# Optimization experiments

Measured on AMD Instinct MI355X. Metric: run time of the kernel, lower is better.

## Reference

```python
import jax, jax.numpy as jnp
import numpy as np

B, H, L, D = 2, 16, 2048, 128


def setup_inputs() -> dict:
    key = jax.random.key(0)
    kq, kk, kv = jax.random.split(key, 3)
    q = jax.random.normal(kq, (B, H, L, D), dtype=jnp.float32)
    k = jax.random.normal(kk, (B, H, L, D), dtype=jnp.float32)
    v = jax.random.normal(kv, (B, H, L, D), dtype=jnp.float32)
    return {"q": q, "k": k, "v": v}


def reference(q, k, v):
    # Causal prefill attention (flash_attn_varlen_func / SDPA is_causal=True path).
    # q, k, v: [B, H, L, D]; scale = 1/sqrt(D) as in the fallback and constructor.
    Lq = q.shape[2]
    Dh = q.shape[3]
    scale = 1.0 / jnp.sqrt(jnp.asarray(Dh, q.dtype))
    scores = jnp.einsum('bhqd,bhkd->bhqk', q, k) * scale  # [B,H,Lq,Lk]
    causal = jnp.tril(jnp.ones((Lq, Lq), dtype=bool))      # [Lq,Lk]
    scores = jnp.where(causal, scores, jnp.finfo(q.dtype).min)
    probs = jax.nn.softmax(scores, axis=-1)
    return jnp.einsum('bhqk,bhkd->bhqd', probs, v)          # [B,H,Lq,D]
```

## Files before the change

### kernel.cpp

```cpp
#include <hip/hip_runtime.h>
#include <hip/hip_bf16.h>
#include <stdint.h>


#define BB 2
#define HH 16
#define LL 2048
#define DD 128

typedef float f32x4 __attribute__((ext_vector_type(4)));
typedef __bf16 bf16x8 __attribute__((ext_vector_type(8)));
typedef __bf16 bf16x2t __attribute__((ext_vector_type(2)));

union Frag16 {
    uint4    u;
    bf16x8   b;
    uint16_t s[8];
    uint32_t w32[4];
};

__device__ inline uint32_t pk2bf(float x, float y) {
    bf16x2t v;
    v.x = (__bf16)x;
    v.y = (__bf16)y;
    return __builtin_bit_cast(uint32_t, v);
}

__device__ inline uint16_t f2bf(float x) {
    uint32_t u = __builtin_bit_cast(uint32_t, x);
    u += 0x7fffu + ((u >> 16) & 1u);
    return (uint16_t)(u >> 16);
}

__device__ inline float fast_exp2(float x) {
#if __has_builtin(__builtin_amdgcn_exp2f)
    return __builtin_amdgcn_exp2f(x);
#else
    return exp2f(x);
#endif
}

__constant__ uint8_t QT[32] = {
    31, 16,  1, 14,   18, 29, 12,  3,    4, 11, 26, 21,    9,  6, 23, 24,
     0, 15, 30, 17,   13,  2, 19, 28,   27, 20,  5, 10,   22, 25,  8,  7};

__global__ __launch_bounds__(256) void conv_kv(
    const float* __restrict__ Kg, const float* __restrict__ Vg,
    uint4* __restrict__ Kf, uint4* __restrict__ Vf)
{
    const int bid = blockIdx.x;
    const int t   = threadIdx.x;
    if (bid < 2048) {
        const int unit = bid;
        #pragma unroll
        for (int i = 0; i < 2; ++i) {
            const int local = t + i * 256;
            const int tile  = unit * 2 + (local >> 8);
            const int c     = local & 255;
            const int ds = c >> 6, quad = (c >> 4) & 3, n16 = c & 15;
            const float* p = Kg + ((size_t)tile * 16 + n16) * DD + ds * 32 + quad * 8;
            float4 a = *(const float4*)p;
            float4 b = *(const float4*)(p + 4);
            Frag16 f;
            f.w32[0] = pk2bf(a.x, a.y); f.w32[1] = pk2bf(a.z, a.w);
            f.w32[2] = pk2bf(b.x, b.y); f.w32[3] = pk2bf(b.z, b.w);
            Kf[(size_t)tile * 256 + c] = f.u;
        }
    } else {
        const int g = bid - 2048;
        const int n16 = t & 15, dt = (t >> 4) & 7, quadH = t >> 7;
        #pragma unroll
        for (int qi = 0; qi < 2; ++qi) {
            const int quad = quadH + 2 * qi;
            const float* base = Vg + ((size_t)g * 32 + quad * 8) * DD + dt * 16 + n16;
            float v[8];
            #pragma unroll
            for (int j = 0; j < 8; ++j) v[j] = base[(size_t)j * DD];
            Frag16 f;
            f.w32[0] = pk2bf(v[0], v[1]); f.w32[1] = pk2bf(v[2], v[3]);
            f.w32[2] = pk2bf(v[4], v[5]); f.w32[3] = pk2bf(v[6], v[7]);
            Vf[(size_t)g * 512 + dt * 64 + quad * 16 + n16] = f.u;
        }
    }
}

__global__ __launch_bounds__(256, 2) void fa_main(
    const float* __restrict__ Qg, const uint4* __restrict__ Kf,
    const uint4* __restrict__ Vf, float* __restrict__ Og)
{
    __shared__ __align__(16) uint16_t Plds[4][16 * 72];

    const int tid  = threadIdx.x;
    const int lane = tid & 63;
    const int w    = tid >> 6;
    const int n16  = lane & 15;
    const int quad = lane >> 4;

    const int i     = blockIdx.x;
    const int xcd   = i & 7;
    const int j     = i >> 3;
    const int k4    = j & 3;
    const int bh_lo = (j >> 2) & 3;
    const int hi    = (j >> 4) & 1;
    const int a4    = j >> 5;
    const int qtile = QT[hi * 16 + a4 * 4 + k4];
    const int bh    = xcd * 4 + bh_lo;

    constexpr float kC   = 0.08838834764831845f * 1.4426950408889634f;
    constexpr float kOff = -16.0f * 1.4426950408889634f;

    const uint4* kpb = Kf + (size_t)(bh * 128) * 256 + lane;
    const uint4* vpb = Vf + (size_t)(bh * 64) * 512 + lane;
    float* Oh = Og + (size_t)bh * LL * DD;

    const int q0     = qtile * 64;
    const int q_base = q0 + w * 16;

    Frag16 qf[4];
    {
        const float* qrow = Qg + ((size_t)bh * LL + q_base + n16) * DD;
        #pragma unroll
        for (int ds = 0; ds < 4; ++ds) {
            const int d0 = ds * 32 + quad * 8;
            float4 a = *(const float4*)(qrow + d0);
            float4 b = *(const float4*)(qrow + d0 + 4);
            qf[ds].w32[0] = pk2bf(a.x, a.y); qf[ds].w32[1] = pk2bf(a.z, a.w);
            qf[ds].w32[2] = pk2bf(b.x, b.y); qf[ds].w32[3] = pk2bf(b.z, b.w);
        }
    }

    f32x4 oacc[8];
    #pragma unroll
    for (int dt = 0; dt < 8; ++dt) oacc[dt] = (f32x4)0.0f;
    float lpart = 0.0f;

    const int ntiles = qtile + 1;

    for (int t = 0; t < ntiles; ++t) {
        const int kv0 = t << 6;
        const uint4* kp = kpb + (size_t)(kv0 >> 4) * 256;
        const uint4* vp = vpb + (size_t)(kv0 >> 5) * 512;

        f32x4 sacc[4] = {(f32x4)0.0f, (f32x4)0.0f, (f32x4)0.0f, (f32x4)0.0f};
        {
            Frag16 kf[2][4];
            #pragma unroll
            for (int kt = 0; kt < 2; ++kt)
                #pragma unroll
                for (int ds = 0; ds < 4; ++ds) kf[kt][ds].u = kp[kt * 256 + ds * 64];
            __builtin_amdgcn_s_setprio(1);
            #pragma unroll
            for (int ds = 0; ds < 4; ++ds) {
                sacc[0] = __builtin_amdgcn_mfma_f32_16x16x32_bf16(kf[0][ds].b, qf[ds].b, sacc[0], 0, 0, 0);
                sacc[1] = __builtin_amdgcn_mfma_f32_16x16x32_bf16(kf[1][ds].b, qf[ds].b, sacc[1], 0, 0, 0);
            }
            __builtin_amdgcn_s_setprio(0);
            #pragma unroll
            for (int kt = 0; kt < 2; ++kt)
                #pragma unroll
                for (int ds = 0; ds < 4; ++ds) kf[kt][ds].u = kp[(kt + 2) * 256 + ds * 64];
            __builtin_amdgcn_s_setprio(1);
            #pragma unroll
            for (int ds = 0; ds < 4; ++ds) {
                sacc[2] = __builtin_amdgcn_mfma_f32_16x16x32_bf16(kf[0][ds].b, qf[ds].b, sacc[2], 0, 0, 0);
                sacc[3] = __builtin_amdgcn_mfma_f32_16x16x32_bf16(kf[1][ds].b, qf[ds].b, sacc[3], 0, 0, 0);
            }
            __builtin_amdgcn_s_setprio(0);
        }

        Frag16 vf[2][8];
        #pragma unroll
        for (int h = 0; h < 2; ++h)
            #pragma unroll
            for (int dt = 0; dt < 8; ++dt) vf[h][dt].u = vp[h * 512 + dt * 64];

        if (kv0 + 63 > q_base) {
            const int qg_ = q_base + n16;
            #pragma unroll
            for (int kt = 0; kt < 4; ++kt) {
                const int kvg = kv0 + kt * 16 + quad * 4;
                #pragma unroll
                for (int r = 0; r < 4; ++r)
                    if (kvg + r > qg_) sacc[kt][r] = -1e30f;
            }
        }

        #pragma unroll
        for (int kt = 0; kt < 4; ++kt) {
            float p0 = fast_exp2(fmaf(sacc[kt][0], kC, kOff));
            float p1 = fast_exp2(fmaf(sacc[kt][1], kC, kOff));
            float p2 = fast_exp2(fmaf(sacc[kt][2], kC, kOff));
            float p3 = fast_exp2(fmaf(sacc[kt][3], kC, kOff));
            lpart += (p0 + p1) + (p2 + p3);
            uint2 pw;
            pw.x = pk2bf(p0, p1);
            pw.y = pk2bf(p2, p3);
            *(uint2*)&Plds[w][n16 * 72 + kt * 16 + quad * 4] = pw;
        }

        #pragma unroll
        for (int h = 0; h < 2; ++h) {
            Frag16 pf;
            pf.u = *(const uint4*)&Plds[w][n16 * 72 + h * 32 + quad * 8];
            __builtin_amdgcn_s_setprio(1);
            #pragma unroll
            for (int dt = 0; dt < 8; ++dt)
                oacc[dt] = __builtin_amdgcn_mfma_f32_16x16x32_bf16(
                    pf.b, vf[h][dt].b, oacc[dt], 0, 0, 0);
            __builtin_amdgcn_s_setprio(0);
        }
    }

    float lsum = lpart;
    lsum += __shfl_xor(lsum, 16);
    lsum += __shfl_xor(lsum, 32);
    #pragma unroll
    for (int r = 0; r < 4; ++r) {
        const float inv = 1.0f / __shfl(lsum, quad * 4 + r);
        float* orow = Oh + (size_t)(q_base + quad * 4 + r) * DD + n16;
        #pragma unroll
        for (int dt = 0; dt < 8; ++dt)
            orow[dt * 16] = oacc[dt][r] * inv;
    }
}

__global__ __launch_bounds__(256) void fa_fallback(
    const float* __restrict__ Qg, const float* __restrict__ Kg,
    const float* __restrict__ Vg, float* __restrict__ Og)
{
    __shared__ uint4 Klds[32 * 16];
    __shared__ uint4 Vlds[128 * 4];
    __shared__ __align__(16) uint16_t Plds[4][32 * 40];

    const int tid  = threadIdx.x;
    const int lane = tid & 63;
    const int w    = tid >> 6;
    const int n16  = lane & 15;
    const int quad = lane >> 4;

    const int bh     = blockIdx.y;
    const int q0     = (gridDim.x - 1 - blockIdx.x) * 128;
    const int q_base = q0 + w * 32;

    const size_t base = (size_t)bh * LL * DD;
    const float* Qh = Qg + base;
    const float* Kh = Kg + base;
    const float* Vh = Vg + base;
    float*       Oh = Og + base;

    constexpr float kC = 0.08838834764831845f * 1.4426950408889634f;

    Frag16 qf[2][4];
    #pragma unroll
    for (int qt = 0; qt < 2; ++qt) {
        const float* qrow = Qh + (size_t)(q_base + qt * 16 + n16) * DD;
        #pragma unroll
        for (int ds = 0; ds < 4; ++ds) {
            const int d0 = ds * 32 + quad * 8;
            float4 a = *(const float4*)(qrow + d0);
            float4 b = *(const float4*)(qrow + d0 + 4);
            Frag16 f;
            f.s[0] = f2bf(a.x); f.s[1] = f2bf(a.y); f.s[2] = f2bf(a.z); f.s[3] = f2bf(a.w);
            f.s[4] = f2bf(b.x); f.s[5] = f2bf(b.y); f.s[6] = f2bf(b.z); f.s[7] = f2bf(b.w);
            qf[qt][ds] = f;
        }
    }

    f32x4 oacc[2][8];
    #pragma unroll
    for (int qt = 0; qt < 2; ++qt)
        #pragma unroll
        for (int dt = 0; dt < 8; ++dt) oacc[qt][dt] = (f32x4)0.0f;
    float mrow[2] = {-1e30f, -1e30f};
    float lrow[2] = {0.0f, 0.0f};

    const int ntiles = q0 / 32 + 4;

    for (int t = 0; t < ntiles; ++t) {
        const int kv0 = t * 32;
        __syncthreads();
        #pragma unroll
        for (int iu = 0; iu < 2; ++iu) {
            const int cid = tid + iu * 256;
            const int r = cid >> 4, c = cid & 15;
            const float* src = Kh + (size_t)(kv0 + r) * DD + c * 8;
            float4 a = *(const float4*)src;
            float4 b = *(const float4*)(src + 4);
            Frag16 f;
            f.s[0] = f2bf(a.x); f.s[1] = f2bf(a.y); f.s[2] = f2bf(a.z); f.s[3] = f2bf(a.w);
            f.s[4] = f2bf(b.x); f.s[5] = f2bf(b.y); f.s[6] = f2bf(b.z); f.s[7] = f2bf(b.w);
            Klds[r * 16 + (c ^ (r & 7))] = f.u;
        }
        #pragma unroll
        for (int iu = 0; iu < 2; ++iu) {
            const int cid = tid + iu * 256;
            const int d = cid >> 2, ch = cid & 3;
            const float* src = Vh + (size_t)(kv0 + ch * 8) * DD + d;
            Frag16 f;
            #pragma unroll
            for (int j = 0; j < 8; ++j) f.s[j] = f2bf(src[(size_t)j * DD]);
            Vlds[d * 4 + (ch ^ ((d >> 1) & 3))] = f.u;
        }
        __syncthreads();

        if (kv0 > q_base + 31) continue;

        f32x4 sacc[2][2];
        #pragma unroll
        for (int kt = 0; kt < 2; ++kt)
            #pragma unroll
            for (int qt = 0; qt < 2; ++qt) sacc[kt][qt] = (f32x4)0.0f;

        #pragma unroll
        for (int ds = 0; ds < 4; ++ds) {
            Frag16 kfr[2];
            #pragma unroll
            for (int kt = 0; kt < 2; ++kt) {
                const int r = kt * 16 + n16;
                const int c = ds * 4 + quad;
                kfr[kt].u = Klds[r * 16 + (c ^ (r & 7))];
            }
            #pragma unroll
            for (int kt = 0; kt < 2; ++kt)
                #pragma unroll
                for (int qt = 0; qt < 2; ++qt)
                    sacc[kt][qt] = __builtin_amdgcn_mfma_f32_16x16x32_bf16(
                        kfr[kt].b, qf[qt][ds].b, sacc[kt][qt], 0, 0, 0);
        }

        if (kv0 + 31 > q_base) {
            #pragma unroll
            for (int kt = 0; kt < 2; ++kt) {
                const int kvg = kv0 + kt * 16 + quad * 4;
                #pragma unroll
                for (int qt = 0; qt < 2; ++qt) {
                    const int qg_ = q_base + qt * 16 + n16;
                    #pragma unroll
                    for (int r = 0; r < 4; ++r)
                        if (kvg + r > qg_) sacc[kt][qt][r] = -1e30f;
                }
            }
        }

        #pragma unroll
        for (int qt = 0; qt < 2; ++qt) {
            float mt = sacc[0][qt][0];
            #pragma unroll
            for (int kt = 0; kt < 2; ++kt)
                #pragma unroll
                for (int r = 0; r < 4; ++r) mt = fmaxf(mt, sacc[kt][qt][r]);
            mt = fmaxf(mt, __shfl_xor(mt, 16));
            mt = fmaxf(mt, __shfl_xor(mt, 32));
            const float mnew  = fmaxf(mrow[qt], mt);
            const float alpha = exp2f((mrow[qt] - mnew) * kC);
            mrow[qt] = mnew;

            float ls = 0.0f;
            uint16_t* prow = &Plds[w][(qt * 16 + n16) * 40];
            #pragma unroll
            for (int kt = 0; kt < 2; ++kt)
                #pragma unroll
                for (int r = 0; r < 4; ++r) {
                    const float p = exp2f((sacc[kt][qt][r] - mnew) * kC);
                    ls += p;
                    prow[kt * 16 + quad * 4 + r] = f2bf(p);
                }
            ls += __shfl_xor(ls, 16);
            ls += __shfl_xor(ls, 32);
            lrow[qt] = lrow[qt] * alpha + ls;

            #pragma unroll
            for (int r = 0; r < 4; ++r) {
                const float ar = __shfl(alpha, quad * 4 + r);
                #pragma unroll
                for (int dt = 0; dt < 8; ++dt) oacc[qt][dt][r] *= ar;
            }
        }

        Frag16 pfr[2];
        #pragma unroll
        for (int qt = 0; qt < 2; ++qt)
            pfr[qt].u = *(const uint4*)&Plds[w][(qt * 16 + n16) * 40 + quad * 8];
        #pragma unroll
        for (int dt = 0; dt < 8; ++dt) {
            const int d = dt * 16 + n16;
            Frag16 vfr;
            vfr.u = Vlds[d * 4 + (quad ^ ((d >> 1) & 3))];
            #pragma unroll
            for (int qt = 0; qt < 2; ++qt)
                oacc[qt][dt] = __builtin_amdgcn_mfma_f32_16x16x32_bf16(
                    pfr[qt].b, vfr.b, oacc[qt][dt], 0, 0, 0);
        }
    }

    #pragma unroll
    for (int qt = 0; qt < 2; ++qt) {
        #pragma unroll
        for (int r = 0; r < 4; ++r) {
            const float lr  = __shfl(lrow[qt], quad * 4 + r);
            const float inv = 1.0f / lr;
            const int row = q_base + qt * 16 + quad * 4 + r;
            float* orow = Oh + (size_t)row * DD + n16;
            #pragma unroll
            for (int dt = 0; dt < 8; ++dt)
                orow[dt * 16] = oacc[qt][dt][r] * inv;
        }
    }
}

extern "C" void kernel_launch(void* const* d_in, const int* in_sizes, int n_in,
                              void* d_out, int out_size, void* d_ws, size_t ws_size,
                              hipStream_t stream) {
    const float* q = (const float*)d_in[0];
    const float* k = (const float*)d_in[1];
    const float* v = (const float*)d_in[2];
    float* o = (float*)d_out;

    const size_t TENS = (size_t)BB * HH * LL * DD * 2;
    if (ws_size >= 2 * TENS) {
        uint4* Kf = (uint4*)d_ws;
        uint4* Vf = (uint4*)((char*)d_ws + TENS);
        conv_kv<<<dim3(4096), dim3(256), 0, stream>>>(k, v, Kf, Vf);
        fa_main<<<dim3(1024), dim3(256), 0, stream>>>(q, Kf, Vf, o);
    } else {
        fa_fallback<<<dim3(16, BB * HH), dim3(256), 0, stream>>>(q, k, v, o);
    }
}
```

Before: 208.1 us.

## Split KV range across wave pairs and pair causal q-tiles for balance

Each block now handles two 32-row query tiles, pair and 63-pair, so causal work is balanced per block. This replaces the QT permutation table. Within a tile, two waves split the KV tiles odd/even and merge partial outputs and row sums through shared memory before the final write. The goal is better load balance and shorter per-wave serial KV loops, at the cost of extra LDS traffic, two barriers per phase, and smaller 32-wide KV steps.

```diff
diff --git a/kernel.cpp b/kernel.cpp
--- a/kernel.cpp
+++ b/kernel.cpp
@@ -39,10 +39,6 @@
     return exp2f(x);
 #endif
 }
-
-__constant__ uint8_t QT[32] = {
-    31, 16,  1, 14,   18, 29, 12,  3,    4, 11, 26, 21,    9,  6, 23, 24,
-     0, 15, 30, 17,   13,  2, 19, 28,   27, 20,  5, 10,   22, 25,  8,  7};
 
 __global__ __launch_bounds__(256) void conv_kv(
     const float* __restrict__ Kg, const float* __restrict__ Vg,
@@ -88,23 +84,23 @@
     const float* __restrict__ Qg, const uint4* __restrict__ Kf,
     const uint4* __restrict__ Vf, float* __restrict__ Og)
 {
-    __shared__ __align__(16) uint16_t Plds[4][16 * 72];
-
-    const int tid  = threadIdx.x;
-    const int lane = tid & 63;
-    const int w    = tid >> 6;
-    const int n16  = lane & 15;
-    const int quad = lane >> 4;
+    __shared__ __align__(16) uint16_t Plds[4][16 * 40];
+    __shared__ float Obuf[2][16 * 132];
+    __shared__ float Lbuf[2][16];
+
+    const int tid   = threadIdx.x;
+    const int lane  = tid & 63;
+    const int w     = tid >> 6;
+    const int n16   = lane & 15;
+    const int quad  = lane >> 4;
+    const int qhalf = w & 1;
+    const int kvway = w >> 1;
 
     const int i     = blockIdx.x;
     const int xcd   = i & 7;
     const int j     = i >> 3;
-    const int k4    = j & 3;
-    const int bh_lo = (j >> 2) & 3;
-    const int hi    = (j >> 4) & 1;
-    const int a4    = j >> 5;
-    const int qtile = QT[hi * 16 + a4 * 4 + k4];
-    const int bh    = xcd * 4 + bh_lo;
+    const int pair  = j & 31;
+    const int bh    = xcd * 4 + (j >> 5);
 
     constexpr float kC   = 0.08838834764831845f * 1.4426950408889634f;
     constexpr float kOff = -16.0f * 1.4426950408889634f;
@@ -113,36 +109,38 @@
     const uint4* vpb = Vf + (size_t)(bh * 64) * 512 + lane;
     float* Oh = Og + (size_t)bh * LL * DD;
 
-    const int q0     = qtile * 64;
-    const int q_base = q0 + w * 16;
-
-    Frag16 qf[4];
-    {
-        const float* qrow = Qg + ((size_t)bh * LL + q_base + n16) * DD;
-        #pragma unroll
-        for (int ds = 0; ds < 4; ++ds) {
-            const int d0 = ds * 32 + quad * 8;
-            float4 a = *(const float4*)(qrow + d0);
-            float4 b = *(const float4*)(qrow + d0 + 4);
-            qf[ds].w32[0] = pk2bf(a.x, a.y); qf[ds].w32[1] = pk2bf(a.z, a.w);
-            qf[ds].w32[2] = pk2bf(b.x, b.y); qf[ds].w32[3] = pk2bf(b.z, b.w);
-        }
-    }
-
-    f32x4 oacc[8];
     #pragma unroll
-    for (int dt = 0; dt < 8; ++dt) oacc[dt] = (f32x4)0.0f;
-    float lpart = 0.0f;
-
-    const int ntiles = qtile + 1;
-
-    for (int t = 0; t < ntiles; ++t) {
-        const int kv0 = t << 6;
-        const uint4* kp = kpb + (size_t)(kv0 >> 4) * 256;
-        const uint4* vp = vpb + (size_t)(kv0 >> 5) * 512;
-
-        f32x4 sacc[4] = {(f32x4)0.0f, (f32x4)0.0f, (f32x4)0.0f, (f32x4)0.0f};
+    for (int phase = 0; phase < 2; ++phase) {
+        const int P32    = phase ? 63 - pair : pair;
+        const int q0     = P32 * 32;
+        const int q_base = q0 + qhalf * 16;
+
+        Frag16 qf[4];
         {
+            const float* qrow = Qg + ((size_t)bh * LL + q_base + n16) * DD;
+            #pragma unroll
+            for (int ds = 0; ds < 4; ++ds) {
+                const int d0 = ds * 32 + quad * 8;
+                float4 a = *(const float4*)(qrow + d0);
+                float4 b = *(const float4*)(qrow + d0 + 4);
+                qf[ds].w32[0] = pk2bf(a.x, a.y); qf[ds].w32[1] = pk2bf(a.z, a.w);
+                qf[ds].w32[2] = pk2bf(b.x, b.y); qf[ds].w32[3] = pk2bf(b.z, b.w);
+            }
+        }
+
+        f32x4 oacc[8];
+        #pragma unroll
+        for (int dt = 0; dt < 8; ++dt) oacc[dt] = (f32x4)0.0f;
+        float lpart = 0.0f;
+
+        const int nt = P32 + 1;
+
+        for (int t = kvway; t < nt; t += 2) {
+            const int kv0 = t << 5;
+            const uint4* kp = kpb + (size_t)(t * 2) * 256;
+            const uint4* vp = vpb + (size_t)t * 512;
+
+            f32x4 sacc[2] = {(f32x4)0.0f, (f32x4)0.0f};
             Frag16 kf[2][4];
             #pragma unroll
             for (int kt = 0; kt < 2; ++kt)
@@ -155,72 +153,71 @@
                 sacc[1] = __builtin_amdgcn_mfma_f32_16x16x32_bf16(kf[1][ds].b, qf[ds].b, sacc[1], 0, 0, 0);
             }
             __builtin_amdgcn_s_setprio(0);
-            #pragma unroll
-            for (int kt = 0; kt < 2; ++kt)
-                #pragma unroll
-                for (int ds = 0; ds < 4; ++ds) kf[kt][ds].u = kp[(kt + 2) * 256 + ds * 64];
-            __builtin_amdgcn_s_setprio(1);
-            #pragma unroll
-            for (int ds = 0; ds < 4; ++ds) {
-                sacc[2] = __builtin_amdgcn_mfma_f32_16x16x32_bf16(kf[0][ds].b, qf[ds].b, sacc[2], 0, 0, 0);
-                sacc[3] = __builtin_amdgcn_mfma_f32_16x16x32_bf16(kf[1][ds].b, qf[ds].b, sacc[3], 0, 0, 0);
-            }
-            __builtin_amdgcn_s_setprio(0);
-        }
-
-        Frag16 vf[2][8];
-        #pragma unroll
-        for (int h = 0; h < 2; ++h)
-            #pragma unroll
-            for (int dt = 0; dt < 8; ++dt) vf[h][dt].u = vp[h * 512 + dt * 64];
-
-        if (kv0 + 63 > q_base) {
-            const int qg_ = q_base + n16;
-            #pragma unroll
-            for (int kt = 0; kt < 4; ++kt) {
-                const int kvg = kv0 + kt * 16 + quad * 4;
-                #pragma unroll
-                for (int r = 0; r < 4; ++r)
-                    if (kvg + r > qg_) sacc[kt][r] = -1e30f;
-            }
-        }
-
-        #pragma unroll
-        for (int kt = 0; kt < 4; ++kt) {
-            float p0 = fast_exp2(fmaf(sacc[kt][0], kC, kOff));
-            float p1 = fast_exp2(fmaf(sacc[kt][1], kC, kOff));
-            float p2 = fast_exp2(fmaf(sacc[kt][2], kC, kOff));
-            float p3 = fast_exp2(fmaf(sacc[kt][3], kC, kOff));
-            lpart += (p0 + p1) + (p2 + p3);
-            uint2 pw;
-            pw.x = pk2bf(p0, p1);
-            pw.y = pk2bf(p2, p3);
-            *(uint2*)&Plds[w][n16 * 72 + kt * 16 + quad * 4] = pw;
-        }
-
-        #pragma unroll
-        for (int h = 0; h < 2; ++h) {
+
+            Frag16 vf[8];
+            #pragma unroll
+            for (int dt = 0; dt < 8; ++dt) vf[dt].u = vp[dt * 64];
+
+            if (kv0 + 31 > q_base) {
+                const int qg_ = q_base + n16;
+                #pragma unroll
+                for (int kt = 0; kt < 2; ++kt) {
+                    const int kvg = kv0 + kt * 16 + quad * 4;
+                    #pragma unroll
+                    for (int r = 0; r < 4; ++r)
+                        if (kvg + r > qg_) sacc[kt][r] = -1e30f;
+                }
+            }
+
+            #pragma unroll
+            for (int kt = 0; kt < 2; ++kt) {
+                float p0 = fast_exp2(fmaf(sacc[kt][0], kC, kOff));
+                float p1 = fast_exp2(fmaf(sacc[kt][1], kC, kOff));
+                float p2 = fast_exp2(fmaf(sacc[kt][2], kC, kOff));
+                float p3 = fast_exp2(fmaf(sacc[kt][3], kC, kOff));
+                lpart += (p0 + p1) + (p2 + p3);
+                uint2 pw;
+                pw.x = pk2bf(p0, p1);
+                pw.y = pk2bf(p2, p3);
+                *(uint2*)&Plds[w][n16 * 40 + kt * 16 + quad * 4] = pw;
+            }
+
             Frag16 pf;
-            pf.u = *(const uint4*)&Plds[w][n16 * 72 + h * 32 + quad * 8];
+            pf.u = *(const uint4*)&Plds[w][n16 * 40 + quad * 8];
             __builtin_amdgcn_s_setprio(1);
             #pragma unroll
             for (int dt = 0; dt < 8; ++dt)
                 oacc[dt] = __builtin_amdgcn_mfma_f32_16x16x32_bf16(
-                    pf.b, vf[h][dt].b, oacc[dt], 0, 0, 0);
+                    pf.b, vf[dt].b, oacc[dt], 0, 0, 0);
             __builtin_amdgcn_s_setprio(0);
         }
-    }
-
-    float lsum = lpart;
-    lsum += __shfl_xor(lsum, 16);
-    lsum += __shfl_xor(lsum, 32);
-    #pragma unroll
-    for (int r = 0; r < 4; ++r) {
-        const float inv = 1.0f / __shfl(lsum, quad * 4 + r);
-        float* orow = Oh + (size_t)(q_base + quad * 4 + r) * DD + n16;
-        #pragma unroll
-        for (int dt = 0; dt < 8; ++dt)
-            orow[dt * 16] = oacc[dt][r] * inv;
+
+        float lsum = lpart;
+        lsum += __shfl_xor(lsum, 16);
+        lsum += __shfl_xor(lsum, 32);
+
+        if (kvway == 1) {
+            if (lane < 16) Lbuf[qhalf][lane] = lsum;
+            #pragma unroll
+            for (int dt = 0; dt < 8; ++dt)
+                #pragma unroll
+                for (int r = 0; r < 4; ++r)
+                    Obuf[qhalf][(quad * 4 + r) * 132 + dt * 16 + n16] = oacc[dt][r];
+        }
+        __syncthreads();
+        if (kvway == 0) {
+            lsum += Lbuf[qhalf][n16];
+            #pragma unroll
+            for (int r = 0; r < 4; ++r) {
+                const float inv = 1.0f / __shfl(lsum, quad * 4 + r);
+                const float* obr = &Obuf[qhalf][(quad * 4 + r) * 132 + n16];
+                float* orow = Oh + (size_t)(q_base + quad * 4 + r) * DD + n16;
+                #pragma unroll
+                for (int dt = 0; dt < 8; ++dt)
+                    orow[dt * 16] = (oacc[dt][r] + obr[dt * 16]) * inv;
+            }
+        }
+        __syncthreads();
     }
 }
 
```

After: 197.7 us. 5.0% less time.

## Stage K/V tiles into LDS with async double-buffered loads in attention

Applied to the files above, without the earlier changes.

The main attention kernel now copies each 32-key K/V tile into shared memory with global_load_lds, double-buffered across iterations, so the whole block shares one load instead of every wave fetching fragments from global memory. The step shrinks from 64 to 32 keys, and the row-sum is computed by an MFMA against a ones fragment instead of shuffles. Launch bounds go from 2 to 4 blocks per SM, and the V conversion kernel now transposes through shared memory so its global reads are coalesced. This adds per-step barriers and more LDS traffic, and the last-tile handling, where only waves 2-3 run the final compute, is delicate.

```diff
diff --git a/kernel.cpp b/kernel.cpp
--- a/kernel.cpp
+++ b/kernel.cpp
@@ -40,6 +40,12 @@
 #endif
 }
 
+__device__ __forceinline__ void stage16(const uint4* g, uint4* l) {
+    __builtin_amdgcn_global_load_lds(
+        (const __attribute__((address_space(1))) unsigned int*)g,
+        (__attribute__((address_space(3))) unsigned int*)l, 16, 0, 0);
+}
+
 __constant__ uint8_t QT[32] = {
     31, 16,  1, 14,   18, 29, 12,  3,    4, 11, 26, 21,    9,  6, 23, 24,
      0, 15, 30, 17,   13,  2, 19, 28,   27, 20,  5, 10,   22, 25,  8,  7};
@@ -48,6 +54,7 @@
     const float* __restrict__ Kg, const float* __restrict__ Vg,
     uint4* __restrict__ Kf, uint4* __restrict__ Vf)
 {
+    __shared__ uint16_t T[32 * 136];
     const int bid = blockIdx.x;
     const int t   = threadIdx.x;
     if (bid < 2048) {
@@ -68,27 +75,42 @@
         }
     } else {
         const int g = bid - 2048;
-        const int n16 = t & 15, dt = (t >> 4) & 7, quadH = t >> 7;
-        #pragma unroll
-        for (int qi = 0; qi < 2; ++qi) {
-            const int quad = quadH + 2 * qi;
-            const float* base = Vg + ((size_t)g * 32 + quad * 8) * DD + dt * 16 + n16;
-            float v[8];
-            #pragma unroll
-            for (int j = 0; j < 8; ++j) v[j] = base[(size_t)j * DD];
+        const float* Vsrc = Vg + (size_t)g * 32 * DD;
+        const int row = t >> 3;
+        const int cg  = (t & 7) * 16;
+        #pragma unroll
+        for (int k = 0; k < 4; ++k) {
+            float4 a = *(const float4*)(Vsrc + (size_t)row * DD + cg + k * 4);
+            uint2 pw;
+            pw.x = pk2bf(a.x, a.y);
+            pw.y = pk2bf(a.z, a.w);
+            *(uint2*)&T[row * 136 + cg + k * 4] = pw;
+        }
+        __syncthreads();
+        #pragma unroll
+        for (int e2 = 0; e2 < 2; ++e2) {
+            const int e   = t + e2 * 256;
+            const int dt  = e >> 6;
+            const int rem = e & 63;
+            const int qd  = rem >> 4;
+            const int nn  = rem & 15;
+            const int col = dt * 16 + nn;
             Frag16 f;
-            f.w32[0] = pk2bf(v[0], v[1]); f.w32[1] = pk2bf(v[2], v[3]);
-            f.w32[2] = pk2bf(v[4], v[5]); f.w32[3] = pk2bf(v[6], v[7]);
-            Vf[(size_t)g * 512 + dt * 64 + quad * 16 + n16] = f.u;
-        }
-    }
-}
-
-__global__ __launch_bounds__(256, 2) void fa_main(
+            #pragma unroll
+            for (int jj = 0; jj < 8; ++jj)
+                f.s[jj] = T[(qd * 8 + jj) * 136 + col];
+            Vf[(size_t)g * 512 + e] = f.u;
+        }
+    }
+}
+
+__global__ __launch_bounds__(256, 4) void fa_main(
     const float* __restrict__ Qg, const uint4* __restrict__ Kf,
     const uint4* __restrict__ Vf, float* __restrict__ Og)
 {
-    __shared__ __align__(16) uint16_t Plds[4][16 * 72];
+    __shared__ __align__(16) uint4 Klds[2][512];
+    __shared__ __align__(16) uint4 Vlds[2][512];
+    __shared__ __align__(16) uint16_t Plds[4][16 * 40];
 
     const int tid  = threadIdx.x;
     const int lane = tid & 63;
@@ -109,16 +131,18 @@
     constexpr float kC   = 0.08838834764831845f * 1.4426950408889634f;
     constexpr float kOff = -16.0f * 1.4426950408889634f;
 
-    const uint4* kpb = Kf + (size_t)(bh * 128) * 256 + lane;
-    const uint4* vpb = Vf + (size_t)(bh * 64) * 512 + lane;
     float* Oh = Og + (size_t)bh * LL * DD;
 
-    const int q0     = qtile * 64;
-    const int q_base = q0 + w * 16;
+    Frag16 onesf;
+    #pragma unroll
+    for (int z = 0; z < 8; ++z) onesf.s[z] = 0x3F80;
+
+    const int q0  = qtile * 64;
+    const int qw0 = q0 + w * 16;
 
     Frag16 qf[4];
     {
-        const float* qrow = Qg + ((size_t)bh * LL + q_base + n16) * DD;
+        const float* qrow = Qg + ((size_t)bh * LL + qw0 + n16) * DD;
         #pragma unroll
         for (int ds = 0; ds < 4; ++ds) {
             const int d0 = ds * 32 + quad * 8;
@@ -132,92 +156,103 @@
     f32x4 oacc[8];
     #pragma unroll
     for (int dt = 0; dt < 8; ++dt) oacc[dt] = (f32x4)0.0f;
-    float lpart = 0.0f;
-
-    const int ntiles = qtile + 1;
-
-    for (int t = 0; t < ntiles; ++t) {
-        const int kv0 = t << 6;
-        const uint4* kp = kpb + (size_t)(kv0 >> 4) * 256;
-        const uint4* vp = vpb + (size_t)(kv0 >> 5) * 512;
-
-        f32x4 sacc[4] = {(f32x4)0.0f, (f32x4)0.0f, (f32x4)0.0f, (f32x4)0.0f};
-        {
-            Frag16 kf[2][4];
-            #pragma unroll
-            for (int kt = 0; kt < 2; ++kt)
-                #pragma unroll
-                for (int ds = 0; ds < 4; ++ds) kf[kt][ds].u = kp[kt * 256 + ds * 64];
+    f32x4 lacc = (f32x4)0.0f;
+
+    const int ns = 2 * qtile + 2;
+
+    const uint4* sg = (w < 2 ? Kf + (size_t)(bh * 128) * 256
+                             : Vf + (size_t)(bh * 64) * 512)
+                      + (w & 1) * 256 + lane;
+    uint4* ldb = (w < 2 ? &Klds[0][0] : &Vlds[0][0]) + (w & 1) * 256;
+
+    auto STAGE = [&](int buf) {
+        uint4* ld = ldb + buf * 512;
+        #pragma unroll
+        for (int c = 0; c < 4; ++c) stage16(sg + c * 64, ld + c * 64);
+        sg += 512;
+    };
+
+    auto COMPUTE = [&](int buf, bool masked, int kv0) {
+        const uint4* Kl = &Klds[buf][0] + lane;
+        const uint4* Vl = &Vlds[buf][0] + lane;
+        f32x4 sacc[2];
+        sacc[0] = (f32x4)0.0f; sacc[1] = (f32x4)0.0f;
+        #pragma unroll
+        for (int kt = 0; kt < 2; ++kt) {
+            Frag16 kfr[4];
+            #pragma unroll
+            for (int ds = 0; ds < 4; ++ds) kfr[ds].u = Kl[kt * 256 + ds * 64];
             __builtin_amdgcn_s_setprio(1);
             #pragma unroll
-            for (int ds = 0; ds < 4; ++ds) {
-                sacc[0] = __builtin_amdgcn_mfma_f32_16x16x32_bf16(kf[0][ds].b, qf[ds].b, sacc[0], 0, 0, 0);
-                sacc[1] = __builtin_amdgcn_mfma_f32_16x16x32_bf16(kf[1][ds].b, qf[ds].b, sacc[1], 0, 0, 0);
-            }
+            for (int ds = 0; ds < 4; ++ds)
+                sacc[kt] = __builtin_amdgcn_mfma_f32_16x16x32_bf16(
+                    kfr[ds].b, qf[ds].b, sacc[kt], 0, 0, 0);
             __builtin_amdgcn_s_setprio(0);
-            #pragma unroll
-            for (int kt = 0; kt < 2; ++kt)
-                #pragma unroll
-                for (int ds = 0; ds < 4; ++ds) kf[kt][ds].u = kp[(kt + 2) * 256 + ds * 64];
-            __builtin_amdgcn_s_setprio(1);
-            #pragma unroll
-            for (int ds = 0; ds < 4; ++ds) {
-                sacc[2] = __builtin_amdgcn_mfma_f32_16x16x32_bf16(kf[0][ds].b, qf[ds].b, sacc[2], 0, 0, 0);
-                sacc[3] = __builtin_amdgcn_mfma_f32_16x16x32_bf16(kf[1][ds].b, qf[ds].b, sacc[3], 0, 0, 0);
-            }
-            __builtin_amdgcn_s_setprio(0);
-        }
-
-        Frag16 vf[2][8];
-        #pragma unroll
-        for (int h = 0; h < 2; ++h)
-            #pragma unroll
-            for (int dt = 0; dt < 8; ++dt) vf[h][dt].u = vp[h * 512 + dt * 64];
-
-        if (kv0 + 63 > q_base) {
-            const int qg_ = q_base + n16;
-            #pragma unroll
-            for (int kt = 0; kt < 4; ++kt) {
+        }
+        if (masked) {
+            const int qg_ = qw0 + n16;
+            #pragma unroll
+            for (int kt = 0; kt < 2; ++kt) {
                 const int kvg = kv0 + kt * 16 + quad * 4;
                 #pragma unroll
                 for (int r = 0; r < 4; ++r)
                     if (kvg + r > qg_) sacc[kt][r] = -1e30f;
             }
         }
-
-        #pragma unroll
-        for (int kt = 0; kt < 4; ++kt) {
+        uint16_t* pw = &Plds[w][n16 * 40];
+        #pragma unroll
+        for (int kt = 0; kt < 2; ++kt) {
             float p0 = fast_exp2(fmaf(sacc[kt][0], kC, kOff));
             float p1 = fast_exp2(fmaf(sacc[kt][1], kC, kOff));
             float p2 = fast_exp2(fmaf(sacc[kt][2], kC, kOff));
             float p3 = fast_exp2(fmaf(sacc[kt][3], kC, kOff));
-            lpart += (p0 + p1) + (p2 + p3);
-            uint2 pw;
-            pw.x = pk2bf(p0, p1);
-            pw.y = pk2bf(p2, p3);
-            *(uint2*)&Plds[w][n16 * 72 + kt * 16 + quad * 4] = pw;
-        }
-
-        #pragma unroll
-        for (int h = 0; h < 2; ++h) {
-            Frag16 pf;
-            pf.u = *(const uint4*)&Plds[w][n16 * 72 + h * 32 + quad * 8];
+            uint2 pw2;
+            pw2.x = pk2bf(p0, p1);
+            pw2.y = pk2bf(p2, p3);
+            *(uint2*)&pw[kt * 16 + quad * 4] = pw2;
+        }
+        Frag16 pf;
+        pf.u = *(const uint4*)&Plds[w][n16 * 40 + quad * 8];
+        __builtin_amdgcn_s_setprio(1);
+        lacc = __builtin_amdgcn_mfma_f32_16x16x32_bf16(pf.b, onesf.b, lacc, 0, 0, 0);
+        __builtin_amdgcn_s_setprio(0);
+        #pragma unroll
+        for (int half = 0; half < 2; ++half) {
+            Frag16 vf[4];
+            #pragma unroll
+            for (int dt = 0; dt < 4; ++dt)
+                vf[dt].u = Vl[(half * 4 + dt) * 64];
             __builtin_amdgcn_s_setprio(1);
             #pragma unroll
-            for (int dt = 0; dt < 8; ++dt)
-                oacc[dt] = __builtin_amdgcn_mfma_f32_16x16x32_bf16(
-                    pf.b, vf[h][dt].b, oacc[dt], 0, 0, 0);
+            for (int dt = 0; dt < 4; ++dt)
+                oacc[half * 4 + dt] = __builtin_amdgcn_mfma_f32_16x16x32_bf16(
+                    pf.b, vf[dt].b, oacc[half * 4 + dt], 0, 0, 0);
             __builtin_amdgcn_s_setprio(0);
         }
-    }
-
-    float lsum = lpart;
-    lsum += __shfl_xor(lsum, 16);
-    lsum += __shfl_xor(lsum, 32);
+    };
+
+    STAGE(0);
+    __syncthreads();
+
+    int cur = 0;
+    for (int t = 0; t < ns - 2; ++t) {
+        STAGE(cur ^ 1);
+        COMPUTE(cur, false, 0);
+        __syncthreads();
+        cur ^= 1;
+    }
+    {
+        STAGE(cur ^ 1);
+        COMPUTE(cur, true, (ns - 2) << 5);
+        __syncthreads();
+        cur ^= 1;
+    }
+    if (w >= 2) COMPUTE(cur, true, (ns - 1) << 5);
+
     #pragma unroll
     for (int r = 0; r < 4; ++r) {
-        const float inv = 1.0f / __shfl(lsum, quad * 4 + r);
-        float* orow = Oh + (size_t)(q_base + quad * 4 + r) * DD + n16;
+        const float inv = 1.0f / lacc[r];
+        float* orow = Oh + (size_t)(qw0 + quad * 4 + r) * DD + n16;
         #pragma unroll
         for (int dt = 0; dt < 8; ++dt)
             orow[dt * 16] = oacc[dt][r] * inv;
```

Result: faster. 173.1 us (-16.8%).
